# Performance work log

Hardware: AMD Instinct MI355X
Metric: run time of the kernel (lower is better)

The kernel has to match this reference:

```python
import jax, jax.numpy as jnp
import numpy as np

Q, N, K, D, H = 1000, 50000, 5, 16, 256
B, S = 4096, 512
IN = D + 1 + D + (K - 1)  # update-network input dim = 37
ABILITY_SCALE = 1.0


def setup_inputs() -> dict:
    key = jax.random.key(0)
    ks = jax.random.split(key, 12)
    theta_embed = jax.random.normal(ks[0], (N + 1, D), dtype=jnp.float32).at[0].set(0.0)
    alpha_raw = 0.1 * jax.random.normal(ks[1], (Q + 1, D), dtype=jnp.float32)
    beta_base = 0.05 * jax.random.normal(ks[2], (Q + 1, 1), dtype=jnp.float32)
    beta_gaps = jnp.full((Q + 1, K - 2), 0.3, dtype=jnp.float32)
    W_h = 0.01 * jax.random.normal(ks[3], (IN, H), dtype=jnp.float32)
    b_h = jnp.zeros((H,), jnp.float32)
    W_g = 0.01 * jax.random.normal(ks[4], (H, D), dtype=jnp.float32)
    b_g = jnp.full((D,), -2.0, jnp.float32)
    W_d = 0.01 * jax.random.normal(ks[5], (H, D), dtype=jnp.float32)
    b_d = jnp.zeros((D,), jnp.float32)
    student_ids = jax.random.randint(ks[6], (B, S), 0, N)
    questions = jax.random.randint(ks[7], (B, S), 0, Q)
    responses = jax.random.randint(ks[8], (B, S), 0, K)
    return dict(theta_embed=theta_embed, alpha_raw=alpha_raw, beta_base=beta_base,
                beta_gaps=beta_gaps, W_h=W_h, b_h=b_h, W_g=W_g, b_g=b_g,
                W_d=W_d, b_d=b_d, student_ids=student_ids, questions=questions,
                responses=responses)


def reference(theta_embed, alpha_raw, beta_base, beta_gaps, W_h, b_h, W_g, b_g,
              W_d, b_d, student_ids, questions, responses):
    cat_vals = jnp.arange(K, dtype=jnp.float32)
    # Item params for all (B, S) positions at once.
    alpha = jnp.exp(0.3 * alpha_raw[questions])                       # (B,S,D)
    sp_gaps = jax.nn.softplus(beta_gaps[questions])                   # (B,S,K-2)
    zero = jnp.zeros(questions.shape + (1,), jnp.float32)
    beta = beta_base[questions] + jnp.concatenate([zero, jnp.cumsum(sp_gaps, -1)], -1)  # (B,S,K-1)

    theta0 = theta_embed[student_ids[:, 0]] * ABILITY_SCALE           # (B,D)

    def step(theta, inp):
        a_t, b_t, r_t = inp                                           # (B,D),(B,K-1),(B,)
        z = jnp.sum(a_t * theta, axis=-1, keepdims=True)              # (B,1)
        logits = jnp.concatenate([jnp.zeros_like(z), jnp.cumsum(z - b_t, -1)], -1)  # (B,K)
        probs = jax.nn.softmax(logits, axis=-1)
        expected = probs @ cat_vals                                   # (B,)
        surprise = r_t - expected
        u = jnp.concatenate([theta, surprise[:, None], a_t, b_t], -1)  # (B,IN)
        h = jnp.tanh(u @ W_h + b_h)
        gate = jax.nn.sigmoid(h @ W_g + b_g)
        delta = jnp.tanh(h @ W_d + b_d)
        return theta + gate * delta, (theta, logits, probs)

    xs = (alpha.transpose(1, 0, 2), beta.transpose(1, 0, 2),
          responses.T.astype(jnp.float32))
    _, (thetas, logits, probs) = jax.lax.scan(step, theta0, xs)
    theta_out = thetas.transpose(1, 0, 2)                             # (B,S,D)
    logits = logits.transpose(1, 0, 2)                                # (B,S,K)
    probs = probs.transpose(1, 0, 2)                                  # (B,S,K)
    return theta_out, alpha, beta, logits, probs
```

## Files before the change

kernel.cpp:

```cpp
#include <hip/hip_runtime.h>
#include <cstddef>
#include <cstdint>


namespace {
constexpr int Bn = 4096;
constexpr int Sn = 512;
constexpr int Qn = 1000;

constexpr int UST = 144;
constexpr int HST = 528;

typedef __attribute__((ext_vector_type(8))) __bf16 bf16x8;
typedef __attribute__((ext_vector_type(4))) float f32x4;
typedef __attribute__((ext_vector_type(4))) unsigned short u16x4;

__device__ __forceinline__ float frcp(float x) { return __builtin_amdgcn_rcpf(x); }
__device__ __forceinline__ float fexp2(float x) {
  float r;
  asm("v_exp_f32 %0, %1" : "=v"(r) : "v"(x));
  return r;
}
__device__ __forceinline__ float ftanh(float x) {
  return 1.0f - 2.0f * frcp(fexp2(x * 2.88539008177793f) + 1.0f);
}
__device__ __forceinline__ float fsigmoid(float x) {
  return frcp(1.0f + fexp2(x * -1.44269504088896f));
}
__device__ __forceinline__ float fsoftplus(float x) {
  return (x > 20.0f) ? x : log1pf(__expf(x));
}
__device__ __forceinline__ unsigned short f2b(float x) {
  return __builtin_bit_cast(unsigned short, (__bf16)x);
}
__device__ __forceinline__ int permk(int k) {
  if (k < 16) return k;
  if (k < 32) return k + 1;
  if (k == 32) return 16;
  return k;
}

#define WAVE_FENCE() asm volatile("s_waitcnt lgkmcnt(0)" ::: "memory")
#define BLOCK_SYNC()                                        \
  do {                                                      \
    asm volatile("s_waitcnt lgkmcnt(0)" ::: "memory");      \
    __builtin_amdgcn_s_barrier();                           \
    asm volatile("" ::: "memory");                          \
  } while (0)

__global__ void precompute_kernel(const float* __restrict__ alpha_raw,
                                  const float* __restrict__ beta_base,
                                  const float* __restrict__ beta_gaps,
                                  float* __restrict__ alpha_q,
                                  float* __restrict__ beta_q) {
  int tid = blockIdx.x * 256 + threadIdx.x;
  if (tid < (Qn + 1) * 16) alpha_q[tid] = __expf(0.3f * alpha_raw[tid]);
  if (tid < Qn + 1) {
    float base = beta_base[tid];
    float sp0 = fsoftplus(beta_gaps[tid * 3 + 0]);
    float sp1 = fsoftplus(beta_gaps[tid * 3 + 1]);
    float sp2 = fsoftplus(beta_gaps[tid * 3 + 2]);
    beta_q[tid * 4 + 0] = base;
    beta_q[tid * 4 + 1] = base + sp0;
    beta_q[tid * 4 + 2] = base + sp0 + sp1;
    beta_q[tid * 4 + 3] = base + sp0 + sp1 + sp2;
  }
}

__global__ void itemout_kernel(const int* __restrict__ questions,
                               const float4* __restrict__ alpha_q4,
                               const float4* __restrict__ beta_q4,
                               float4* __restrict__ out_alpha4,
                               float4* __restrict__ out_beta4) {
  int tid = blockIdx.x * 256 + threadIdx.x;
  int pos = tid >> 2, j = tid & 3;
  if (pos >= Bn * Sn) return;
  int q = questions[pos];
  out_alpha4[(size_t)pos * 4 + j] = alpha_q4[(size_t)q * 4 + j];
  if (j == 0) out_beta4[pos] = beta_q4[q];
}

__global__ __launch_bounds__(256, 1) void scan_kernel(
    const float* __restrict__ theta_embed,
    const float* __restrict__ W_h, const float* __restrict__ b_h,
    const float* __restrict__ W_g, const float* __restrict__ b_g,
    const float* __restrict__ W_d, const float* __restrict__ b_d,
    const int* __restrict__ student_ids, const int* __restrict__ questions,
    const int* __restrict__ responses,
    const float* __restrict__ alpha_q, const float4* __restrict__ beta_q4,
    float* __restrict__ out_theta, float* __restrict__ out_logits,
    float* __restrict__ out_probs) {
  __shared__ char sU[4 * 16 * UST];
  __shared__ char sH[2 * 16 * HST];

  const int tid = threadIdx.x;
  const int lane = tid & 63;
  const int wv = tid >> 6;
  const int s = lane & 15;
  const int g = lane >> 4;
  const int bs = blockIdx.x * 16 + s;

  char* uB = sU + wv * (16 * UST);
  {
    int4 zz = {0, 0, 0, 0};
    char* p = uB + (lane >> 2) * UST + (lane & 3) * 32;
    *(int4*)p = zz;
    *(int4*)(p + 16) = zz;
  }

  bf16x8 whA[4][2];
#pragma unroll
  for (int m = 0; m < 4; ++m) {
    const int j = 64 * wv + 16 * m + s;
#pragma unroll
    for (int kk = 0; kk < 2; ++kk) {
#pragma unroll
      for (int e = 0; e < 8; ++e) {
        const int k = kk * 32 + g * 8 + e;
        float v = 0.0f;
        if (k < 37) v = W_h[permk(k) * 256 + j];
        whA[m][kk][e] = (__bf16)v;
      }
    }
  }
  bf16x8 wgdA[2][8];
#pragma unroll
  for (int m = 0; m < 2; ++m) {
    const float* Wm = m ? W_d : W_g;
#pragma unroll
    for (int kk = 0; kk < 8; ++kk) {
#pragma unroll
      for (int e = 0; e < 8; ++e) {
        const int k = kk * 32 + g * 8 + e;
        wgdA[m][kk][e] = (__bf16)Wm[k * 16 + s];
      }
    }
  }
  f32x4 bias_h[4];
#pragma unroll
  for (int m = 0; m < 4; ++m)
    bias_h[m] = *(const f32x4*)(b_h + 64 * wv + 16 * m + 4 * g);
  const f32x4 bias_g = *(const f32x4*)(b_g + 4 * g);
  const f32x4 bias_d = *(const f32x4*)(b_d + 4 * g);
  const f32x4 zero4 = {0.0f, 0.0f, 0.0f, 0.0f};

  const int* qrow = questions + (size_t)bs * Sn;
  const int* rrow = responses + (size_t)bs * Sn;

  f32x4 th = *(const f32x4*)(theta_embed +
                             (size_t)student_ids[(size_t)bs * Sn] * 16 + 4 * g);

  int r = rrow[0];
  int q0 = qrow[0];
  float4 a4 = *(const float4*)(alpha_q + (size_t)q0 * 16 + 4 * g);
  float4 bq = beta_q4[q0];
  int qn = qrow[1], rn = rrow[1];

#pragma unroll 2
  for (int t = 0; t < Sn; ++t) {
    const float4 a4n = *(const float4*)(alpha_q + (size_t)qn * 16 + 4 * g);
    const float4 bqn = beta_q4[qn];
    const int t2 = (t + 2 < Sn) ? t + 2 : Sn - 1;
    const int qn2 = qrow[t2];
    const int rn2 = rrow[t2];

    float zp = a4.x * th.x + a4.y * th.y + a4.z * th.z + a4.w * th.w;
    zp += __shfl_xor(zp, 16);
    zp += __shfl_xor(zp, 32);
    const float z = zp;

    const float l1 = z - bq.x;
    const float l2 = l1 + z - bq.y;
    const float l3 = l2 + z - bq.z;
    const float l4 = l3 + z - bq.w;
    const float m = fmaxf(fmaxf(fmaxf(l1, l2), fmaxf(l3, l4)), 0.0f);
    const float e0 = fexp2(-m * 1.44269504088896f);
    const float e1 = fexp2((l1 - m) * 1.44269504088896f);
    const float e2 = fexp2((l2 - m) * 1.44269504088896f);
    const float e3 = fexp2((l3 - m) * 1.44269504088896f);
    const float e4 = fexp2((l4 - m) * 1.44269504088896f);
    const float inv = frcp(e0 + e1 + e2 + e3 + e4);
    const float expected = (e1 + 2.0f * e2 + 3.0f * e3 + 4.0f * e4) * inv;
    const float surprise = (float)r - expected;

    if (wv == (t & 3)) {
      const size_t pos = (size_t)bs * Sn + t;
      *(f32x4*)(out_theta + pos * 16 + 4 * g) = th;
      const float lv = (g == 0) ? 0.0f : (g == 1) ? l1 : (g == 2) ? l2 : l3;
      const float pv = ((g == 0) ? e0 : (g == 1) ? e1 : (g == 2) ? e2 : e3) * inv;
      out_logits[pos * 5 + g] = lv;
      out_probs[pos * 5 + g] = pv;
      if (g == 3) {
        out_logits[pos * 5 + 4] = l4;
        out_probs[pos * 5 + 4] = e4 * inv;
      }
    }

    {
      char* ur = uB + s * UST;
      u16x4 thb = {f2b(th.x), f2b(th.y), f2b(th.z), f2b(th.w)};
      *(u16x4*)(ur + 8 * g) = thb;
      u16x4 ab = {f2b(a4.x), f2b(a4.y), f2b(a4.z), f2b(a4.w)};
      *(u16x4*)(ur + 32 + 8 * g) = ab;
      if (g == 0) {
        u16x4 sb = {f2b(surprise), f2b(bq.x), f2b(bq.y), f2b(bq.z)};
        *(u16x4*)(ur + 64) = sb;
        *(unsigned short*)(ur + 72) = f2b(bq.w);
      }
    }
    WAVE_FENCE();

    const bf16x8 ub0 = *(const bf16x8*)(uB + s * UST + 16 * g);
    const bf16x8 ub1 = *(const bf16x8*)(uB + s * UST + 64 + 16 * g);
    f32x4 acc0 = __builtin_amdgcn_mfma_f32_16x16x32_bf16(whA[0][0], ub0, bias_h[0], 0, 0, 0);
    f32x4 acc1 = __builtin_amdgcn_mfma_f32_16x16x32_bf16(whA[1][0], ub0, bias_h[1], 0, 0, 0);
    f32x4 acc2 = __builtin_amdgcn_mfma_f32_16x16x32_bf16(whA[2][0], ub0, bias_h[2], 0, 0, 0);
    f32x4 acc3 = __builtin_amdgcn_mfma_f32_16x16x32_bf16(whA[3][0], ub0, bias_h[3], 0, 0, 0);
    acc0 = __builtin_amdgcn_mfma_f32_16x16x32_bf16(whA[0][1], ub1, acc0, 0, 0, 0);
    acc1 = __builtin_amdgcn_mfma_f32_16x16x32_bf16(whA[1][1], ub1, acc1, 0, 0, 0);
    acc2 = __builtin_amdgcn_mfma_f32_16x16x32_bf16(whA[2][1], ub1, acc2, 0, 0, 0);
    acc3 = __builtin_amdgcn_mfma_f32_16x16x32_bf16(whA[3][1], ub1, acc3, 0, 0, 0);

    char* hB = sH + (t & 1) * (16 * HST);
    {
      char* hr = hB + s * HST + 128 * wv + 8 * g;
      u16x4 h0 = {f2b(ftanh(acc0.x)), f2b(ftanh(acc0.y)), f2b(ftanh(acc0.z)), f2b(ftanh(acc0.w))};
      *(u16x4*)(hr) = h0;
      u16x4 h1 = {f2b(ftanh(acc1.x)), f2b(ftanh(acc1.y)), f2b(ftanh(acc1.z)), f2b(ftanh(acc1.w))};
      *(u16x4*)(hr + 32) = h1;
      u16x4 h2 = {f2b(ftanh(acc2.x)), f2b(ftanh(acc2.y)), f2b(ftanh(acc2.z)), f2b(ftanh(acc2.w))};
      *(u16x4*)(hr + 64) = h2;
      u16x4 h3 = {f2b(ftanh(acc3.x)), f2b(ftanh(acc3.y)), f2b(ftanh(acc3.z)), f2b(ftanh(acc3.w))};
      *(u16x4*)(hr + 96) = h3;
    }
    BLOCK_SYNC();

    const char* hr = hB + s * HST + 16 * g;
    f32x4 ag0 = bias_g, ad0 = bias_d, ag1 = zero4, ad1 = zero4;
#pragma unroll
    for (int kk = 0; kk < 4; ++kk) {
      const bf16x8 hb = *(const bf16x8*)(hr + 64 * kk);
      ag0 = __builtin_amdgcn_mfma_f32_16x16x32_bf16(wgdA[0][kk], hb, ag0, 0, 0, 0);
      ad0 = __builtin_amdgcn_mfma_f32_16x16x32_bf16(wgdA[1][kk], hb, ad0, 0, 0, 0);
    }
#pragma unroll
    for (int kk = 4; kk < 8; ++kk) {
      const bf16x8 hb = *(const bf16x8*)(hr + 64 * kk);
      ag1 = __builtin_amdgcn_mfma_f32_16x16x32_bf16(wgdA[0][kk], hb, ag1, 0, 0, 0);
      ad1 = __builtin_amdgcn_mfma_f32_16x16x32_bf16(wgdA[1][kk], hb, ad1, 0, 0, 0);
    }
    const f32x4 ag = ag0 + ag1;
    const f32x4 ad = ad0 + ad1;
    th.x += fsigmoid(ag.x) * ftanh(ad.x);
    th.y += fsigmoid(ag.y) * ftanh(ad.y);
    th.z += fsigmoid(ag.z) * ftanh(ad.z);
    th.w += fsigmoid(ag.w) * ftanh(ad.w);

    a4 = a4n; bq = bqn; r = rn;
    qn = qn2; rn = rn2;
  }
}

}

extern "C" void kernel_launch(void* const* d_in, const int* in_sizes, int n_in,
                              void* d_out, int out_size, void* d_ws, size_t ws_size,
                              hipStream_t stream) {
  const float* theta_embed = (const float*)d_in[0];
  const float* alpha_raw   = (const float*)d_in[1];
  const float* beta_base   = (const float*)d_in[2];
  const float* beta_gaps   = (const float*)d_in[3];
  const float* W_h = (const float*)d_in[4];
  const float* b_h = (const float*)d_in[5];
  const float* W_g = (const float*)d_in[6];
  const float* b_g = (const float*)d_in[7];
  const float* W_d = (const float*)d_in[8];
  const float* b_d = (const float*)d_in[9];
  const int* student_ids = (const int*)d_in[10];
  const int* questions   = (const int*)d_in[11];
  const int* responses   = (const int*)d_in[12];

  float* out = (float*)d_out;
  float* out_theta  = out;
  float* out_alpha  = out_theta + (size_t)Bn * Sn * 16;
  float* out_beta   = out_alpha + (size_t)Bn * Sn * 16;
  float* out_logits = out_beta  + (size_t)Bn * Sn * 4;
  float* out_probs  = out_logits + (size_t)Bn * Sn * 5;

  float* alpha_q = (float*)d_ws;
  float* beta_q  = alpha_q + (size_t)(Qn + 1) * 16;

  hipLaunchKernelGGL(precompute_kernel, dim3(63), dim3(256), 0, stream,
                     alpha_raw, beta_base, beta_gaps, alpha_q, beta_q);
  hipLaunchKernelGGL(itemout_kernel, dim3((Bn * Sn * 4) / 256), dim3(256), 0, stream,
                     questions, (const float4*)alpha_q, (const float4*)beta_q,
                     (float4*)out_alpha, (float4*)out_beta);
  hipLaunchKernelGGL(scan_kernel, dim3(Bn / 16), dim3(256), 0, stream,
                     theta_embed, W_h, b_h, W_g, b_g, W_d, b_d,
                     student_ids, questions, responses,
                     alpha_q, (const float4*)beta_q,
                     out_theta, out_logits, out_probs);
}
```

Before: 608.3 us.

## Split gate/delta GEMM across waves with LDS partial-sum reduction

Each wave now computes the gate and delta projections only over its own 64-wide slice of the hidden layer, using 4 MFMAs instead of 16. It writes the partial sums to a double-buffered LDS area, and after one barrier every wave adds up the four partials. This cuts redundant MFMA work and register pressure per wave, at the cost of extra LDS traffic and a reduction step. The change also precomputes cumulative beta sums scaled by log2(e), which simplifies the softmax logits. Output stores are spread across waves by output type instead of rotating by timestep.

```diff
diff --git a/kernel.cpp b/kernel.cpp
--- a/kernel.cpp
+++ b/kernel.cpp
@@ -10,6 +10,12 @@
 
 constexpr int UST = 144;
 constexpr int HST = 528;
+constexpr int PLN = 36;
+constexpr int PWV = 64 * PLN;
+constexpr int PBUF = 4 * PWV;
+
+constexpr float LOG2E = 1.44269504088896f;
+constexpr float LN2 = 0.693147180559945f;
 
 typedef __attribute__((ext_vector_type(8))) __bf16 bf16x8;
 typedef __attribute__((ext_vector_type(4))) float f32x4;
@@ -25,7 +31,7 @@
   return 1.0f - 2.0f * frcp(fexp2(x * 2.88539008177793f) + 1.0f);
 }
 __device__ __forceinline__ float fsigmoid(float x) {
-  return frcp(1.0f + fexp2(x * -1.44269504088896f));
+  return frcp(1.0f + fexp2(x * -LOG2E));
 }
 __device__ __forceinline__ float fsoftplus(float x) {
   return (x > 20.0f) ? x : log1pf(__expf(x));
@@ -52,7 +58,8 @@
                                   const float* __restrict__ beta_base,
                                   const float* __restrict__ beta_gaps,
                                   float* __restrict__ alpha_q,
-                                  float* __restrict__ beta_q) {
+                                  float* __restrict__ beta_q,
+                                  float* __restrict__ bsumC_q) {
   int tid = blockIdx.x * 256 + threadIdx.x;
   if (tid < (Qn + 1) * 16) alpha_q[tid] = __expf(0.3f * alpha_raw[tid]);
   if (tid < Qn + 1) {
@@ -60,10 +67,16 @@
     float sp0 = fsoftplus(beta_gaps[tid * 3 + 0]);
     float sp1 = fsoftplus(beta_gaps[tid * 3 + 1]);
     float sp2 = fsoftplus(beta_gaps[tid * 3 + 2]);
-    beta_q[tid * 4 + 0] = base;
-    beta_q[tid * 4 + 1] = base + sp0;
-    beta_q[tid * 4 + 2] = base + sp0 + sp1;
-    beta_q[tid * 4 + 3] = base + sp0 + sp1 + sp2;
+    float b1 = base, b2 = base + sp0, b3 = b2 + sp1, b4 = b3 + sp2;
+    beta_q[tid * 4 + 0] = b1;
+    beta_q[tid * 4 + 1] = b2;
+    beta_q[tid * 4 + 2] = b3;
+    beta_q[tid * 4 + 3] = b4;
+    float c1 = b1, c2 = c1 + b2, c3 = c2 + b3, c4 = c3 + b4;
+    bsumC_q[tid * 4 + 0] = c1 * LOG2E;
+    bsumC_q[tid * 4 + 1] = c2 * LOG2E;
+    bsumC_q[tid * 4 + 2] = c3 * LOG2E;
+    bsumC_q[tid * 4 + 3] = c4 * LOG2E;
   }
 }
 
@@ -88,10 +101,12 @@
     const int* __restrict__ student_ids, const int* __restrict__ questions,
     const int* __restrict__ responses,
     const float* __restrict__ alpha_q, const float4* __restrict__ beta_q4,
+    const float4* __restrict__ bsumC_q4,
     float* __restrict__ out_theta, float* __restrict__ out_logits,
     float* __restrict__ out_probs) {
   __shared__ char sU[4 * 16 * UST];
-  __shared__ char sH[2 * 16 * HST];
+  __shared__ char sH[16 * HST];
+  __shared__ char sP[2 * PBUF];
 
   const int tid = threadIdx.x;
   const int lane = tid & 63;
@@ -123,15 +138,15 @@
       }
     }
   }
-  bf16x8 wgdA[2][8];
+  bf16x8 wgdA[2][2];
 #pragma unroll
   for (int m = 0; m < 2; ++m) {
     const float* Wm = m ? W_d : W_g;
 #pragma unroll
-    for (int kk = 0; kk < 8; ++kk) {
+    for (int kk = 0; kk < 2; ++kk) {
 #pragma unroll
       for (int e = 0; e < 8; ++e) {
-        const int k = kk * 32 + g * 8 + e;
+        const int k = 64 * wv + 32 * kk + 8 * g + e;
         wgdA[m][kk][e] = (__bf16)Wm[k * 16 + s];
       }
     }
@@ -154,12 +169,14 @@
   int q0 = qrow[0];
   float4 a4 = *(const float4*)(alpha_q + (size_t)q0 * 16 + 4 * g);
   float4 bq = beta_q4[q0];
+  float4 bsC = bsumC_q4[q0];
   int qn = qrow[1], rn = rrow[1];
 
 #pragma unroll 2
   for (int t = 0; t < Sn; ++t) {
     const float4 a4n = *(const float4*)(alpha_q + (size_t)qn * 16 + 4 * g);
     const float4 bqn = beta_q4[qn];
+    const float4 bsCn = bsumC_q4[qn];
     const int t2 = (t + 2 < Sn) ? t + 2 : Sn - 1;
     const int qn2 = qrow[t2];
     const int rn2 = rrow[t2];
@@ -167,31 +184,35 @@
     float zp = a4.x * th.x + a4.y * th.y + a4.z * th.z + a4.w * th.w;
     zp += __shfl_xor(zp, 16);
     zp += __shfl_xor(zp, 32);
-    const float z = zp;
-
-    const float l1 = z - bq.x;
-    const float l2 = l1 + z - bq.y;
-    const float l3 = l2 + z - bq.z;
-    const float l4 = l3 + z - bq.w;
-    const float m = fmaxf(fmaxf(fmaxf(l1, l2), fmaxf(l3, l4)), 0.0f);
-    const float e0 = fexp2(-m * 1.44269504088896f);
-    const float e1 = fexp2((l1 - m) * 1.44269504088896f);
-    const float e2 = fexp2((l2 - m) * 1.44269504088896f);
-    const float e3 = fexp2((l3 - m) * 1.44269504088896f);
-    const float e4 = fexp2((l4 - m) * 1.44269504088896f);
+    const float z2 = zp * LOG2E;
+
+    const float lc1 = z2 - bsC.x;
+    const float lc2 = fmaf(2.0f, z2, -bsC.y);
+    const float lc3 = fmaf(3.0f, z2, -bsC.z);
+    const float lc4 = fmaf(4.0f, z2, -bsC.w);
+    const float m = fmaxf(fmaxf(fmaxf(lc1, lc2), fmaxf(lc3, lc4)), 0.0f);
+    const float e0 = fexp2(-m);
+    const float e1 = fexp2(lc1 - m);
+    const float e2 = fexp2(lc2 - m);
+    const float e3 = fexp2(lc3 - m);
+    const float e4 = fexp2(lc4 - m);
     const float inv = frcp(e0 + e1 + e2 + e3 + e4);
     const float expected = (e1 + 2.0f * e2 + 3.0f * e3 + 4.0f * e4) * inv;
     const float surprise = (float)r - expected;
 
-    if (wv == (t & 3)) {
-      const size_t pos = (size_t)bs * Sn + t;
+    const size_t pos = (size_t)bs * Sn + t;
+    if (wv == 0) {
       *(f32x4*)(out_theta + pos * 16 + 4 * g) = th;
-      const float lv = (g == 0) ? 0.0f : (g == 1) ? l1 : (g == 2) ? l2 : l3;
+    } else if (wv == 1) {
+      const float lv =
+          (g == 0) ? 0.0f : (g == 1) ? lc1 * LN2 : (g == 2) ? lc2 * LN2 : lc3 * LN2;
+      out_logits[pos * 5 + g] = lv;
+    } else if (wv == 2) {
       const float pv = ((g == 0) ? e0 : (g == 1) ? e1 : (g == 2) ? e2 : e3) * inv;
-      out_logits[pos * 5 + g] = lv;
       out_probs[pos * 5 + g] = pv;
+    } else {
       if (g == 3) {
-        out_logits[pos * 5 + 4] = l4;
+        out_logits[pos * 5 + 4] = lc4 * LN2;
         out_probs[pos * 5 + 4] = e4 * inv;
       }
     }
@@ -221,9 +242,8 @@
     acc2 = __builtin_amdgcn_mfma_f32_16x16x32_bf16(whA[2][1], ub1, acc2, 0, 0, 0);
     acc3 = __builtin_amdgcn_mfma_f32_16x16x32_bf16(whA[3][1], ub1, acc3, 0, 0, 0);
 
-    char* hB = sH + (t & 1) * (16 * HST);
     {
-      char* hr = hB + s * HST + 128 * wv + 8 * g;
+      char* hr = sH + s * HST + 128 * wv + 8 * g;
       u16x4 h0 = {f2b(ftanh(acc0.x)), f2b(ftanh(acc0.y)), f2b(ftanh(acc0.z)), f2b(ftanh(acc0.w))};
       *(u16x4*)(hr) = h0;
       u16x4 h1 = {f2b(ftanh(acc1.x)), f2b(ftanh(acc1.y)), f2b(ftanh(acc1.z)), f2b(ftanh(acc1.w))};
@@ -233,30 +253,43 @@
       u16x4 h3 = {f2b(ftanh(acc3.x)), f2b(ftanh(acc3.y)), f2b(ftanh(acc3.z)), f2b(ftanh(acc3.w))};
       *(u16x4*)(hr + 96) = h3;
     }
+    WAVE_FENCE();
+
+    const char* hr = sH + s * HST + 128 * wv + 16 * g;
+    const bf16x8 hb0 = *(const bf16x8*)(hr);
+    const bf16x8 hb1 = *(const bf16x8*)(hr + 64);
+    f32x4 pg = __builtin_amdgcn_mfma_f32_16x16x32_bf16(wgdA[0][0], hb0, zero4, 0, 0, 0);
+    f32x4 pd = __builtin_amdgcn_mfma_f32_16x16x32_bf16(wgdA[1][0], hb0, zero4, 0, 0, 0);
+    pg = __builtin_amdgcn_mfma_f32_16x16x32_bf16(wgdA[0][1], hb1, pg, 0, 0, 0);
+    pd = __builtin_amdgcn_mfma_f32_16x16x32_bf16(wgdA[1][1], hb1, pd, 0, 0, 0);
+
+    char* sPp = sP + (t & 1) * PBUF;
+    {
+      char* pp = sPp + wv * PWV + lane * PLN;
+      *(f32x4*)pp = pg;
+      *(f32x4*)(pp + 16) = pd;
+    }
     BLOCK_SYNC();
 
-    const char* hr = hB + s * HST + 16 * g;
-    f32x4 ag0 = bias_g, ad0 = bias_d, ag1 = zero4, ad1 = zero4;
-#pragma unroll
-    for (int kk = 0; kk < 4; ++kk) {
-      const bf16x8 hb = *(const bf16x8*)(hr + 64 * kk);
-      ag0 = __builtin_amdgcn_mfma_f32_16x16x32_bf16(wgdA[0][kk], hb, ag0, 0, 0, 0);
-      ad0 = __builtin_amdgcn_mfma_f32_16x16x32_bf16(wgdA[1][kk], hb, ad0, 0, 0, 0);
-    }
-#pragma unroll
-    for (int kk = 4; kk < 8; ++kk) {
-      const bf16x8 hb = *(const bf16x8*)(hr + 64 * kk);
-      ag1 = __builtin_amdgcn_mfma_f32_16x16x32_bf16(wgdA[0][kk], hb, ag1, 0, 0, 0);
-      ad1 = __builtin_amdgcn_mfma_f32_16x16x32_bf16(wgdA[1][kk], hb, ad1, 0, 0, 0);
-    }
-    const f32x4 ag = ag0 + ag1;
-    const f32x4 ad = ad0 + ad1;
+    f32x4 ag = bias_g + pg;
+    f32x4 ad = bias_d + pd;
+    {
+      const char* p1 = sPp + (((wv + 1) & 3) * PWV) + lane * PLN;
+      const char* p2 = sPp + (((wv + 2) & 3) * PWV) + lane * PLN;
+      const char* p3 = sPp + (((wv + 3) & 3) * PWV) + lane * PLN;
+      ag += *(const f32x4*)p1;
+      ad += *(const f32x4*)(p1 + 16);
+      ag += *(const f32x4*)p2;
+      ad += *(const f32x4*)(p2 + 16);
+      ag += *(const f32x4*)p3;
+      ad += *(const f32x4*)(p3 + 16);
+    }
     th.x += fsigmoid(ag.x) * ftanh(ad.x);
     th.y += fsigmoid(ag.y) * ftanh(ad.y);
     th.z += fsigmoid(ag.z) * ftanh(ad.z);
     th.w += fsigmoid(ag.w) * ftanh(ad.w);
 
-    a4 = a4n; bq = bqn; r = rn;
+    a4 = a4n; bq = bqn; bsC = bsCn; r = rn;
     qn = qn2; rn = rn2;
   }
 }
@@ -289,15 +322,16 @@
 
   float* alpha_q = (float*)d_ws;
   float* beta_q  = alpha_q + (size_t)(Qn + 1) * 16;
+  float* bsumC_q = beta_q + (size_t)(Qn + 1) * 4;
 
   hipLaunchKernelGGL(precompute_kernel, dim3(63), dim3(256), 0, stream,
-                     alpha_raw, beta_base, beta_gaps, alpha_q, beta_q);
+                     alpha_raw, beta_base, beta_gaps, alpha_q, beta_q, bsumC_q);
   hipLaunchKernelGGL(itemout_kernel, dim3((Bn * Sn * 4) / 256), dim3(256), 0, stream,
                      questions, (const float4*)alpha_q, (const float4*)beta_q,
                      (float4*)out_alpha, (float4*)out_beta);
   hipLaunchKernelGGL(scan_kernel, dim3(Bn / 16), dim3(256), 0, stream,
                      theta_embed, W_h, b_h, W_g, b_g, W_d, b_d,
                      student_ids, questions, responses,
-                     alpha_q, (const float4*)beta_q,
+                     alpha_q, (const float4*)beta_q, (const float4*)bsumC_q,
                      out_theta, out_logits, out_probs);
 }
```

Measured after the change: 968.6 us. 1.59x slower.
